# Performance work log

Hardware: AMD Instinct MI355X
Metric: run time of the kernel (lower is better)

Reference implementation:

```python
import jax, jax.numpy as jnp
import numpy as np

RAY_DIR = jnp.array([0.4395064455, 0.617598629942, 0.652231566745], dtype=jnp.float32)
TOL = 1e-7
CONTACT_THRESH = 25.0   # opt.contact_thresh
COLLISION_THRESH = 25.0  # opt.collision_thresh
BIG = 1e10


def mesh_contains(points, triangles, tri_valid):
    """Moller-Trumbore ray casting (fixed ray dir), parity test.
    points [B,P,3], triangles [B,T,3,3], tri_valid [B,T] -> exterior [B,P] bool."""
    v0, v1, v2 = triangles[:, :, 0, :], triangles[:, :, 1, :], triangles[:, :, 2, :]
    e1 = v1 - v0
    e2 = v2 - v0
    pvec = jnp.cross(jnp.broadcast_to(RAY_DIR, e2.shape), e2)          # [B,T,3]
    dets = jnp.sum(e1 * pvec, -1)                                      # [B,T]
    parallel = jnp.abs(dets) < TOL
    invdet = 1.0 / (dets + 0.1 * TOL)
    tvec = points[:, None, :, :] - v0[:, :, None, :]                   # [B,T,P,3]
    u = jnp.sum(tvec * pvec[:, :, None, :], -1) * invdet[:, :, None]   # [B,T,P]
    qvec = jnp.cross(tvec, e1[:, :, None, :])                          # [B,T,P,3]
    v = jnp.sum(qvec * RAY_DIR, -1) * invdet[:, :, None]
    t = jnp.sum(e2[:, :, None, :] * qvec, -1) * invdet[:, :, None]
    inter = (u > 0) & (u < 1) & (v > 0) & (u + v < 1) & (t > TOL)
    inter = inter & (~parallel & tri_valid)[:, :, None]
    n_hits = jnp.sum(inter.astype(jnp.int32), axis=1)                  # [B,P]
    return (n_hits % 2) == 0


def masked_mean_loss(vals, mask):
    m = mask.astype(vals.dtype)
    tot = m.sum()
    loss = jnp.where(tot > 0, (m * vals).sum() / jnp.maximum(tot, 1.0), 0.0)
    row = m.sum(1)
    losses = jnp.where(row > 0, (m * vals).sum(1) / jnp.maximum(row, 1.0), 0.0)
    return loss, losses


def setup_inputs() -> dict:
    key = jax.random.key(0)
    ks = jax.random.split(key, 6)
    B, Nh, Fh, No, Fo = 8, 778, 1538, 2000, 4000
    hand_verts = jax.random.normal(ks[0], (B, Nh, 3), dtype=jnp.float32)
    hand_faces = jax.random.randint(ks[1], (B, Fh, 3), 0, Nh, dtype=jnp.int32)
    obj_verts = jax.random.normal(ks[2], (B, No, 3), dtype=jnp.float32)
    obj_faces = jax.random.randint(ks[3], (B, Fo, 3), 0, 1200, dtype=jnp.int32)
    obj_vert_splits = 1200 + jax.random.randint(ks[4], (B,), 0, No - 1200 + 1, dtype=jnp.int32)
    obj_face_splits = 2400 + jax.random.randint(ks[5], (B,), 0, Fo - 2400 + 1, dtype=jnp.int32)
    return {"hand_verts": hand_verts, "hand_faces": hand_faces,
            "obj_verts": obj_verts, "obj_faces": obj_faces,
            "obj_vert_splits": obj_vert_splits, "obj_face_splits": obj_face_splits}


def reference(hand_verts, hand_faces, obj_verts, obj_faces, obj_vert_splits, obj_face_splits):
    B, Nh, _ = hand_verts.shape
    No = obj_verts.shape[1]
    Fo = obj_faces.shape[1]
    sg = jax.lax.stop_gradient

    # gather triangles (batched)
    hand_tri = jax.vmap(lambda v, f: v[f])(hand_verts, hand_faces)     # [B,Fh,3,3]
    obj_tri = jax.vmap(lambda v, f: v[f])(obj_verts, obj_faces)        # [B,Fo,3,3]

    face_valid = jnp.arange(Fo)[None, :] < obj_face_splits[:, None]    # [B,Fo]
    vert_valid = jnp.arange(No)[None, :] < obj_vert_splits[:, None]    # [B,No]

    # containment tests run on detached geometry (as in original)
    hand_tri_valid = jnp.ones(hand_tri.shape[:2], dtype=bool)
    exterior_obj = mesh_contains(sg(obj_verts), sg(hand_tri), hand_tri_valid)   # [B,No]
    exterior_hand = mesh_contains(sg(hand_verts), sg(obj_tri), face_valid)      # [B,Nh]

    penetr_o_mask = (~exterior_obj) & vert_valid
    penetr_h_mask = ~exterior_hand

    # ragged squared pairwise distances (bmm form of original), padded cols -> BIG
    rx = jnp.sum(hand_verts * hand_verts, -1)                          # [B,Nh]
    ry = jnp.sum(obj_verts * obj_verts, -1)                            # [B,No]
    zz = jnp.einsum('bnd,bmd->bnm', hand_verts, obj_verts)             # [B,Nh,No]
    dists = rx[:, :, None] + ry[:, None, :] - 2.0 * zz
    dists = jnp.where(vert_valid[:, None, :], dists, BIG)

    minoh_idxs = jnp.argmin(dists, axis=1)                             # [B,No]
    minho_idxs = jnp.argmin(dists, axis=2)                             # [B,Nh]

    results_close = jnp.take_along_axis(obj_verts, minho_idxs[:, :, None], axis=1)    # [B,Nh,3]
    results_o_close = jnp.take_along_axis(hand_verts, minoh_idxs[:, :, None], axis=1)  # [B,No,3]

    # contact_target == 'all'
    anchor_dists = jnp.sqrt(jnp.sum((results_close - hand_verts) ** 2, -1))    # [B,Nh]
    anchor_o_dist = jnp.sqrt(jnp.sum((results_o_close - obj_verts) ** 2, -1))  # [B,No]

    # contact_mode == 'dist_tanh' -> below_dist all ones
    contact_vals = CONTACT_THRESH * jnp.tanh(anchor_dists / CONTACT_THRESH)
    # collision_mode == 'dist_tanh'
    collision_vals = COLLISION_THRESH * jnp.tanh(anchor_dists / COLLISION_THRESH)
    collision_o_vals = COLLISION_THRESH * jnp.tanh(anchor_o_dist / COLLISION_THRESH)
    collision_o_vals = jnp.where(vert_valid, collision_o_vals, 0.0)

    # contact_zones == 'all'
    missed_mask = exterior_hand

    missed_loss, missed_losses = masked_mean_loss(contact_vals, missed_mask)
    penetr_h_loss, penetr_h_losses = masked_mean_loss(collision_vals, penetr_h_mask)
    penetr_o_loss, penetr_o_losses = masked_mean_loss(collision_o_vals, penetr_o_mask)
    penetr_loss = penetr_h_loss + penetr_o_loss
    penetr_losses = penetr_h_losses + penetr_o_losses

    return missed_loss, penetr_loss, missed_losses, penetr_losses
```

## Files before the change

### kernel.cpp

```cpp
#include <hip/hip_runtime.h>
#include <hip/hip_bf16.h>


#define RX 0.4395064455f
#define RY 0.617598629942f
#define RZ 0.652231566745f

#define MAXCHUNK_F4 512
#define PTS_PER_BLK 512

struct Params {
    const float* hand_verts; const int* hand_faces;
    const float* obj_verts;  const int* obj_faces;
    const int* ovsplit; const int* ofsplit;
    int* hitsA;
    int* hitsB;
    float* anchor_h; float* anchor_o; float* partials;
    unsigned int* done;
    float* out;
    int B, Nh, Fh, No, Fo;
    int pbA, CA, chunkA, blocksA;
    int pbB, CB, chunkB, blocksB;
};

__device__ __forceinline__ void tri_pre_one(const float* __restrict__ vb,
                                            const int* __restrict__ f,
                                            float4* o) {
#pragma clang fp contract(off)
    int i0 = f[0], i1 = f[1], i2 = f[2];
    float v0x = vb[i0*3+0], v0y = vb[i0*3+1], v0z = vb[i0*3+2];
    float v1x = vb[i1*3+0], v1y = vb[i1*3+1], v1z = vb[i1*3+2];
    float v2x = vb[i2*3+0], v2y = vb[i2*3+1], v2z = vb[i2*3+2];
    float e1x = v1x - v0x, e1y = v1y - v0y, e1z = v1z - v0z;
    float e2x = v2x - v0x, e2y = v2y - v0y, e2z = v2z - v0z;
    float px = RY*e2z - RZ*e2y;
    float py = RZ*e2x - RX*e2z;
    float pz = RX*e2y - RY*e2x;
    float det = (e1x*px + e1y*py) + e1z*pz;
    float invdet = 1.0f / (det + 1e-8f);
    bool valid = !(fabsf(det) < 1e-7f);
    o[0] = make_float4(v0x, v0y, v0z, invdet);
    o[1] = make_float4(e1x, e1y, e1z, valid ? 1.0f : 0.0f);
    o[2] = make_float4(e2x, e2y, e2z, 0.0f);
    o[3] = make_float4(px,  py,  pz,  0.0f);
}

__device__ __forceinline__ int mt_test(float qx, float qy, float qz,
                                       const float4& f0, const float4& f1,
                                       const float4& f2, const float4& f3) {
#pragma clang fp contract(off)
    float tvx = qx - f0.x, tvy = qy - f0.y, tvz = qz - f0.z;
    float u  = ((tvx*f3.x + tvy*f3.y) + tvz*f3.z) * f0.w;
    float qvx = tvy*f1.z - tvz*f1.y;
    float qvy = tvz*f1.x - tvx*f1.z;
    float qvz = tvx*f1.y - tvy*f1.x;
    float v  = ((qvx*RX + qvy*RY) + qvz*RZ) * f0.w;
    float tt = ((f2.x*qvx + f2.y*qvy) + f2.z*qvz) * f0.w;
    bool hit = (u > 0.0f) && (u < 1.0f) && (v > 0.0f) &&
               ((u + v) < 1.0f) && (tt > 1e-7f) && (f1.w != 0.0f);
    return hit ? 1 : 0;
}

__device__ __forceinline__ void raycast_vb(const Params& p, int vbid, int tid,
                                           float4* s_tri) {
#pragma clang fp contract(off)
    const float* pts; const float* tverts; const int* tfaces; int* slots;
    int P, T, Nv, c, pb, b, chunk, tlim, plim;
    if (vbid < p.blocksA) {
        int per_b = p.pbA * p.CA;
        b  = vbid / per_b;
        int r = vbid - b * per_b;
        c  = r / p.pbA;
        pb = r - c * p.pbA;
        pts = p.obj_verts; tverts = p.hand_verts; tfaces = p.hand_faces;
        slots = p.hitsA;
        P = p.No; T = p.Fh; Nv = p.Nh; chunk = p.chunkA;
        tlim = p.Fh; plim = min(p.No, p.ovsplit[b]);
    } else {
        int j = vbid - p.blocksA;
        int per_b = p.pbB * p.CB;
        b  = j / per_b;
        int r = j - b * per_b;
        c  = r / p.pbB;
        pb = r - c * p.pbB;
        pts = p.hand_verts; tverts = p.obj_verts; tfaces = p.obj_faces;
        slots = p.hitsB;
        P = p.Nh; T = p.Fo; Nv = p.No; chunk = p.chunkB;
        tlim = min(p.Fo, p.ofsplit[b]); plim = p.Nh;
    }

    int tStart = c * chunk;
    if (tStart >= tlim) return;
    if (pb * PTS_PER_BLK >= plim) return;
    int nTri = min(tStart + chunk, tlim) - tStart;

    if (tid < nTri) {
        int t = tStart + tid;
        tri_pre_one(tverts + (size_t)b * Nv * 3,
                    tfaces + ((size_t)b * T + t) * 3,
                    s_tri + (size_t)tid * 4);
    }

    int p1 = pb * PTS_PER_BLK + tid;
    int p2 = p1 + 256;
    bool act1 = p1 < plim, act2 = p2 < plim;
    float q1x = 0.f, q1y = 0.f, q1z = 0.f;
    float q2x = 0.f, q2y = 0.f, q2z = 0.f;
    if (act1) {
        const float* q = pts + ((size_t)b * P + p1) * 3;
        q1x = q[0]; q1y = q[1]; q1z = q[2];
    }
    if (act2) {
        const float* q = pts + ((size_t)b * P + p2) * 3;
        q2x = q[0]; q2y = q[1]; q2z = q[2];
    }
    __syncthreads();

    if (!act1) return;
    int cnt1 = 0, cnt2 = 0;
    for (int i = 0; i < nTri; ++i) {
        const float4 f0 = s_tri[(i<<2)+0];
        const float4 f1 = s_tri[(i<<2)+1];
        const float4 f2 = s_tri[(i<<2)+2];
        const float4 f3 = s_tri[(i<<2)+3];
        cnt1 += mt_test(q1x, q1y, q1z, f0, f1, f2, f3);
        cnt2 += mt_test(q2x, q2y, q2z, f0, f1, f2, f3);
    }
    int* base = slots + ((size_t)(c * p.B + b)) * P;
    base[p1] = cnt1;
    if (act2) base[p2] = cnt2;
}

__device__ __forceinline__ void min_one(const Params& p, int w, int lane) {
#pragma clang fp contract(off)
    int nHand = p.B * p.Nh;
    const float* refv; const float* loopv; int loopN; float* outp;
    if (w < nHand) {
        int b = w / p.Nh;
        int n = w - b * p.Nh;
        refv  = p.hand_verts + ((size_t)b * p.Nh + n) * 3;
        loopv = p.obj_verts + (size_t)b * p.No * 3;
        loopN = p.ovsplit[b];
        outp  = p.anchor_h + (size_t)b * p.Nh + n;
    } else {
        int j = w - nHand;
        int b = j / p.No;
        int m = j - b * p.No;
        if (m >= p.ovsplit[b]) return;
        refv  = p.obj_verts + ((size_t)b * p.No + m) * 3;
        loopv = p.hand_verts + (size_t)b * p.Nh * 3;
        loopN = p.Nh;
        outp  = p.anchor_o + (size_t)b * p.No + m;
    }
    float hx = refv[0], hy = refv[1], hz = refv[2];
    float rx = (hx*hx + hy*hy) + hz*hz;
    unsigned long long best = ~0ull;
    for (int m = lane; m < loopN; m += 64) {
        float ox = loopv[m*3+0], oy = loopv[m*3+1], oz = loopv[m*3+2];
        float ry = (ox*ox + oy*oy) + oz*oz;
        float zz = (hx*ox + hy*oy) + hz*oz;
        float d = (rx + ry) - 2.0f * zz;
        unsigned long long e = ((unsigned long long)__float_as_uint(d) << 32) | (unsigned)m;
        if (e < best) best = e;
    }
    for (int off = 32; off > 0; off >>= 1) {
        unsigned long long o = __shfl_xor(best, off, 64);
        if (o < best) best = o;
    }
    if (lane == 0) {
        int idx = (best == ~0ull) ? 0 : (int)(best & 0xffffffffu);
        const float* cv = loopv + (size_t)idx * 3;
        float dx = cv[0] - hx, dy = cv[1] - hy, dz = cv[2] - hz;
        *outp = sqrtf((dx*dx + dy*dy) + dz*dz);
    }
}

__global__ __launch_bounds__(256) void mega(Params p) {
    __shared__ float4 s_tri[MAXCHUNK_F4];
    const int tid = threadIdx.x;
    const int bid = blockIdx.x;
    if (bid == 0 && tid == 0) *p.done = 0u;
    const int nRay = p.blocksA + p.blocksB;
    if (bid < nRay) {
        raycast_vb(p, bid, tid, s_tri);
    } else {
        int w = (bid - nRay) * 4 + (tid >> 6);
        if (w < p.B * (p.Nh + p.No)) min_one(p, w, tid & 63);
    }
}

__global__ __launch_bounds__(1024) void reduce_fin(Params p) {
    const int b = blockIdx.x, tid = threadIdx.x;
    const int wave = tid >> 6, lane = tid & 63;
    float s0=0.f,s1=0.f,s2=0.f,s3=0.f,s4=0.f,s5=0.f;

    int tlimB = min(p.Fo, p.ofsplit[b]);
    int nCB = (tlimB + p.chunkB - 1) / p.chunkB;
    for (int n = tid; n < p.Nh; n += 1024) {
        int par = 0;
        for (int c = 0; c < nCB; ++c)
            par += p.hitsB[((size_t)(c * p.B + b)) * p.Nh + n];
        bool ext = (par & 1) == 0;
        float val = 25.0f * tanhf(p.anchor_h[(size_t)b*p.Nh + n] / 25.0f);
        if (ext) { s0 += val; s1 += 1.0f; } else { s2 += val; s3 += 1.0f; }
    }
    int split = p.ovsplit[b];
    for (int m = tid; m < split; m += 1024) {
        int par = 0;
        for (int c = 0; c < p.CA; ++c)
            par += p.hitsA[((size_t)(c * p.B + b)) * p.No + m];
        if (par & 1) {
            s4 += 25.0f * tanhf(p.anchor_o[(size_t)b*p.No + m] / 25.0f);
            s5 += 1.0f;
        }
    }
    for (int off = 32; off > 0; off >>= 1) {
        s0 += __shfl_xor(s0, off, 64);
        s1 += __shfl_xor(s1, off, 64);
        s2 += __shfl_xor(s2, off, 64);
        s3 += __shfl_xor(s3, off, 64);
        s4 += __shfl_xor(s4, off, 64);
        s5 += __shfl_xor(s5, off, 64);
    }
    __shared__ float red[16][6];
    __shared__ bool s_last;
    if (lane == 0) {
        red[wave][0]=s0; red[wave][1]=s1; red[wave][2]=s2;
        red[wave][3]=s3; red[wave][4]=s4; red[wave][5]=s5;
    }
    __syncthreads();
    if (tid == 0) {
        float t0=0.f,t1=0.f,t2=0.f,t3=0.f,t4=0.f,t5=0.f;
        for (int wv = 0; wv < 16; ++wv) {
            t0 += red[wv][0]; t1 += red[wv][1]; t2 += red[wv][2];
            t3 += red[wv][3]; t4 += red[wv][4]; t5 += red[wv][5];
        }
        p.out[2 + b]  = (t1 > 0.f) ? t0 / fmaxf(t1, 1.f) : 0.f;
        float ph      = (t3 > 0.f) ? t2 / fmaxf(t3, 1.f) : 0.f;
        float po      = (t5 > 0.f) ? t4 / fmaxf(t5, 1.f) : 0.f;
        p.out[10 + b] = ph + po;
        float* pp = p.partials + b * 6;
        pp[0]=t0; pp[1]=t1; pp[2]=t2; pp[3]=t3; pp[4]=t4; pp[5]=t5;
        __threadfence();
        unsigned int old = atomicAdd(p.done, 1u);
        s_last = (old == (unsigned int)(gridDim.x - 1));
    }
    __syncthreads();
    if (!s_last || tid != 0) return;
    __threadfence();
    float sm=0.f,cm=0.f,sph=0.f,cph=0.f,spo=0.f,cpo=0.f;
    for (int bb = 0; bb < p.B; ++bb) {
        const float* pp = p.partials + bb * 6;
        sm  += pp[0]; cm  += pp[1]; sph += pp[2];
        cph += pp[3]; spo += pp[4]; cpo += pp[5];
    }
    float missed = (cm  > 0.f) ? sm  / fmaxf(cm , 1.f) : 0.f;
    float ph     = (cph > 0.f) ? sph / fmaxf(cph, 1.f) : 0.f;
    float po     = (cpo > 0.f) ? spo / fmaxf(cpo, 1.f) : 0.f;
    p.out[0] = missed;
    p.out[1] = ph + po;
}

extern "C" void kernel_launch(void* const* d_in, const int* in_sizes, int n_in,
                              void* d_out, int out_size, void* d_ws, size_t ws_size,
                              hipStream_t stream) {
    Params p;
    p.hand_verts = (const float*)d_in[0];
    p.hand_faces = (const int*)d_in[1];
    p.obj_verts  = (const float*)d_in[2];
    p.obj_faces  = (const int*)d_in[3];
    p.ovsplit    = (const int*)d_in[4];
    p.ofsplit    = (const int*)d_in[5];
    p.out        = (float*)d_out;

    p.B  = in_sizes[4];
    p.Nh = in_sizes[0] / (3 * p.B);
    p.Fh = in_sizes[1] / (3 * p.B);
    p.No = in_sizes[2] / (3 * p.B);
    p.Fo = in_sizes[3] / (3 * p.B);

    p.CA = 16; p.CB = 32;
    p.chunkA = (p.Fh + p.CA - 1) / p.CA;
    p.chunkB = (p.Fo + p.CB - 1) / p.CB;
    p.pbA = (p.No + PTS_PER_BLK - 1) / PTS_PER_BLK;
    p.pbB = (p.Nh + PTS_PER_BLK - 1) / PTS_PER_BLK;
    p.blocksA = p.pbA * p.CA * p.B;
    p.blocksB = p.pbB * p.CB * p.B;

    char* ws = (char*)d_ws;
    size_t off = 0;
    auto alloc = [&](size_t bytes) -> void* {
        void* q = ws + off;
        off = (off + bytes + 255) & ~(size_t)255;
        return q;
    };
    p.hitsA    = (int*)   alloc((size_t)p.CA * p.B * p.No * sizeof(int));
    p.hitsB    = (int*)   alloc((size_t)p.CB * p.B * p.Nh * sizeof(int));
    p.anchor_h = (float*) alloc((size_t)p.B * p.Nh * sizeof(float));
    p.anchor_o = (float*) alloc((size_t)p.B * p.No * sizeof(float));
    p.partials = (float*) alloc((size_t)p.B * 6 * sizeof(float));
    p.done     = (unsigned int*)alloc(sizeof(unsigned int));

    int totalMin   = p.B * (p.Nh + p.No);
    int nMinBlocks = (totalMin + 3) / 4;
    int grid = p.blocksA + p.blocksB + nMinBlocks;

    mega<<<grid, 256, 0, stream>>>(p);
    reduce_fin<<<p.B, 1024, 0, stream>>>(p);
}
```

Before: 133.4 us.

## Fuse reduction into cooperative persistent kernel and retile raycast with more points per thread

Replaces the two-kernel launch with a single cooperative persistent kernel that loops over virtual blocks, then uses grid syncs to run a split per-batch reduction and the final loss computation. The raycast now packs triangle data into three float4s plus one scalar, folding the parallel flag into a zero invdet. Each thread tests four points instead of two, with smaller triangle chunks (more chunks). This is meant to remove a kernel launch and cut shared-memory traffic per triangle. The cost is grid-wide barrier overhead, limits on cooperative occupancy, and a larger partial-hit buffer to reduce.

```diff
diff --git a/kernel.cpp b/kernel.cpp
--- a/kernel.cpp
+++ b/kernel.cpp
@@ -1,13 +1,15 @@
 #include <hip/hip_runtime.h>
-#include <hip/hip_bf16.h>
+#include <hip/hip_cooperative_groups.h>
+
+namespace cg = cooperative_groups;
 
 
 #define RX 0.4395064455f
 #define RY 0.617598629942f
 #define RZ 0.652231566745f
 
-#define MAXCHUNK_F4 512
-#define PTS_PER_BLK 512
+#define MAXCHUNK 128
+#define PTS_PER_BLK 1024
 
 struct Params {
     const float* hand_verts; const int* hand_faces;
@@ -15,17 +17,17 @@
     const int* ovsplit; const int* ofsplit;
     int* hitsA;
     int* hitsB;
-    float* anchor_h; float* anchor_o; float* partials;
-    unsigned int* done;
+    float* anchor_h; float* anchor_o;
+    float* partials;
     float* out;
     int B, Nh, Fh, No, Fo;
-    int pbA, CA, chunkA, blocksA;
-    int pbB, CB, chunkB, blocksB;
+    int chunkA, chunkB, nChA, nChB;
+    int pbA, pbB, blocksA, blocksB, nMinBlk;
 };
 
 __device__ __forceinline__ void tri_pre_one(const float* __restrict__ vb,
                                             const int* __restrict__ f,
-                                            float4* o) {
+                                            float4* o, float* opz) {
 #pragma clang fp contract(off)
     int i0 = f[0], i1 = f[1], i2 = f[2];
     float v0x = vb[i0*3+0], v0y = vb[i0*3+1], v0z = vb[i0*3+2];
@@ -38,36 +40,36 @@
     float pz = RX*e2y - RY*e2x;
     float det = (e1x*px + e1y*py) + e1z*pz;
     float invdet = 1.0f / (det + 1e-8f);
-    bool valid = !(fabsf(det) < 1e-7f);
+    if (fabsf(det) < 1e-7f) invdet = 0.0f;
     o[0] = make_float4(v0x, v0y, v0z, invdet);
-    o[1] = make_float4(e1x, e1y, e1z, valid ? 1.0f : 0.0f);
-    o[2] = make_float4(e2x, e2y, e2z, 0.0f);
-    o[3] = make_float4(px,  py,  pz,  0.0f);
+    o[1] = make_float4(e1x, e1y, e1z, px);
+    o[2] = make_float4(e2x, e2y, e2z, py);
+    *opz = pz;
 }
 
 __device__ __forceinline__ int mt_test(float qx, float qy, float qz,
                                        const float4& f0, const float4& f1,
-                                       const float4& f2, const float4& f3) {
+                                       const float4& f2, float pz) {
 #pragma clang fp contract(off)
     float tvx = qx - f0.x, tvy = qy - f0.y, tvz = qz - f0.z;
-    float u  = ((tvx*f3.x + tvy*f3.y) + tvz*f3.z) * f0.w;
+    float u  = ((tvx*f1.w + tvy*f2.w) + tvz*pz) * f0.w;
     float qvx = tvy*f1.z - tvz*f1.y;
     float qvy = tvz*f1.x - tvx*f1.z;
     float qvz = tvx*f1.y - tvy*f1.x;
     float v  = ((qvx*RX + qvy*RY) + qvz*RZ) * f0.w;
     float tt = ((f2.x*qvx + f2.y*qvy) + f2.z*qvz) * f0.w;
     bool hit = (u > 0.0f) && (u < 1.0f) && (v > 0.0f) &&
-               ((u + v) < 1.0f) && (tt > 1e-7f) && (f1.w != 0.0f);
+               ((u + v) < 1.0f) && (tt > 1e-7f);
     return hit ? 1 : 0;
 }
 
 __device__ __forceinline__ void raycast_vb(const Params& p, int vbid, int tid,
-                                           float4* s_tri) {
+                                           float4* s_tri, float* s_pz) {
 #pragma clang fp contract(off)
     const float* pts; const float* tverts; const int* tfaces; int* slots;
     int P, T, Nv, c, pb, b, chunk, tlim, plim;
     if (vbid < p.blocksA) {
-        int per_b = p.pbA * p.CA;
+        int per_b = p.pbA * p.nChA;
         b  = vbid / per_b;
         int r = vbid - b * per_b;
         c  = r / p.pbA;
@@ -78,7 +80,7 @@
         tlim = p.Fh; plim = min(p.No, p.ovsplit[b]);
     } else {
         int j = vbid - p.blocksA;
-        int per_b = p.pbB * p.CB;
+        int per_b = p.pbB * p.nChB;
         b  = j / per_b;
         int r = j - b * per_b;
         c  = r / p.pbB;
@@ -98,37 +100,37 @@
         int t = tStart + tid;
         tri_pre_one(tverts + (size_t)b * Nv * 3,
                     tfaces + ((size_t)b * T + t) * 3,
-                    s_tri + (size_t)tid * 4);
+                    s_tri + (size_t)tid * 3, s_pz + tid);
     }
 
     int p1 = pb * PTS_PER_BLK + tid;
-    int p2 = p1 + 256;
-    bool act1 = p1 < plim, act2 = p2 < plim;
-    float q1x = 0.f, q1y = 0.f, q1z = 0.f;
-    float q2x = 0.f, q2y = 0.f, q2z = 0.f;
-    if (act1) {
-        const float* q = pts + ((size_t)b * P + p1) * 3;
-        q1x = q[0]; q1y = q[1]; q1z = q[2];
-    }
-    if (act2) {
-        const float* q = pts + ((size_t)b * P + p2) * 3;
-        q2x = q[0]; q2y = q[1]; q2z = q[2];
-    }
+    int p2 = p1 + 256, p3 = p1 + 512, p4 = p1 + 768;
+    bool act1 = p1 < plim, act2 = p2 < plim, act3 = p3 < plim, act4 = p4 < plim;
+    float q1x=0.f,q1y=0.f,q1z=0.f, q2x=0.f,q2y=0.f,q2z=0.f;
+    float q3x=0.f,q3y=0.f,q3z=0.f, q4x=0.f,q4y=0.f,q4z=0.f;
+    if (act1) { const float* q = pts + ((size_t)b*P + p1)*3; q1x=q[0]; q1y=q[1]; q1z=q[2]; }
+    if (act2) { const float* q = pts + ((size_t)b*P + p2)*3; q2x=q[0]; q2y=q[1]; q2z=q[2]; }
+    if (act3) { const float* q = pts + ((size_t)b*P + p3)*3; q3x=q[0]; q3y=q[1]; q3z=q[2]; }
+    if (act4) { const float* q = pts + ((size_t)b*P + p4)*3; q4x=q[0]; q4y=q[1]; q4z=q[2]; }
     __syncthreads();
 
     if (!act1) return;
-    int cnt1 = 0, cnt2 = 0;
+    int c1=0, c2=0, c3=0, c4=0;
     for (int i = 0; i < nTri; ++i) {
-        const float4 f0 = s_tri[(i<<2)+0];
-        const float4 f1 = s_tri[(i<<2)+1];
-        const float4 f2 = s_tri[(i<<2)+2];
-        const float4 f3 = s_tri[(i<<2)+3];
-        cnt1 += mt_test(q1x, q1y, q1z, f0, f1, f2, f3);
-        cnt2 += mt_test(q2x, q2y, q2z, f0, f1, f2, f3);
+        const float4 f0 = s_tri[i*3+0];
+        const float4 f1 = s_tri[i*3+1];
+        const float4 f2 = s_tri[i*3+2];
+        const float pz = s_pz[i];
+        c1 += mt_test(q1x,q1y,q1z, f0,f1,f2,pz);
+        if (act2) c2 += mt_test(q2x,q2y,q2z, f0,f1,f2,pz);
+        if (act3) c3 += mt_test(q3x,q3y,q3z, f0,f1,f2,pz);
+        if (act4) c4 += mt_test(q4x,q4y,q4z, f0,f1,f2,pz);
     }
     int* base = slots + ((size_t)(c * p.B + b)) * P;
-    base[p1] = cnt1;
-    if (act2) base[p2] = cnt2;
+    base[p1] = c1;
+    if (act2) base[p2] = c2;
+    if (act3) base[p3] = c3;
+    if (act4) base[p4] = c4;
 }
 
 __device__ __forceinline__ void min_one(const Params& p, int w, int lane) {
@@ -175,28 +177,16 @@
     }
 }
 
-__global__ __launch_bounds__(256) void mega(Params p) {
-    __shared__ float4 s_tri[MAXCHUNK_F4];
-    const int tid = threadIdx.x;
-    const int bid = blockIdx.x;
-    if (bid == 0 && tid == 0) *p.done = 0u;
-    const int nRay = p.blocksA + p.blocksB;
-    if (bid < nRay) {
-        raycast_vb(p, bid, tid, s_tri);
-    } else {
-        int w = (bid - nRay) * 4 + (tid >> 6);
-        if (w < p.B * (p.Nh + p.No)) min_one(p, w, tid & 63);
-    }
-}
-
-__global__ __launch_bounds__(1024) void reduce_fin(Params p) {
-    const int b = blockIdx.x, tid = threadIdx.x;
+__device__ __forceinline__ void reduce_part(const Params& p, int r, int tid) {
+    const int b    = r >> 2;
     const int wave = tid >> 6, lane = tid & 63;
+    const int wv   = (r & 3) * 4 + wave;
+    const int vt   = wv * 64 + lane;
     float s0=0.f,s1=0.f,s2=0.f,s3=0.f,s4=0.f,s5=0.f;
 
     int tlimB = min(p.Fo, p.ofsplit[b]);
     int nCB = (tlimB + p.chunkB - 1) / p.chunkB;
-    for (int n = tid; n < p.Nh; n += 1024) {
+    for (int n = vt; n < p.Nh; n += 1024) {
         int par = 0;
         for (int c = 0; c < nCB; ++c)
             par += p.hitsB[((size_t)(c * p.B + b)) * p.Nh + n];
@@ -205,9 +195,9 @@
         if (ext) { s0 += val; s1 += 1.0f; } else { s2 += val; s3 += 1.0f; }
     }
     int split = p.ovsplit[b];
-    for (int m = tid; m < split; m += 1024) {
+    for (int m = vt; m < split; m += 1024) {
         int par = 0;
-        for (int c = 0; c < p.CA; ++c)
+        for (int c = 0; c < p.nChA; ++c)
             par += p.hitsA[((size_t)(c * p.B + b)) * p.No + m];
         if (par & 1) {
             s4 += 25.0f * tanhf(p.anchor_o[(size_t)b*p.No + m] / 25.0f);
@@ -222,43 +212,67 @@
         s4 += __shfl_xor(s4, off, 64);
         s5 += __shfl_xor(s5, off, 64);
     }
-    __shared__ float red[16][6];
-    __shared__ bool s_last;
     if (lane == 0) {
-        red[wave][0]=s0; red[wave][1]=s1; red[wave][2]=s2;
-        red[wave][3]=s3; red[wave][4]=s4; red[wave][5]=s5;
-    }
-    __syncthreads();
-    if (tid == 0) {
-        float t0=0.f,t1=0.f,t2=0.f,t3=0.f,t4=0.f,t5=0.f;
-        for (int wv = 0; wv < 16; ++wv) {
-            t0 += red[wv][0]; t1 += red[wv][1]; t2 += red[wv][2];
-            t3 += red[wv][3]; t4 += red[wv][4]; t5 += red[wv][5];
+        float* q = p.partials + ((size_t)(b * 16 + wv)) * 6;
+        q[0]=s0; q[1]=s1; q[2]=s2; q[3]=s3; q[4]=s4; q[5]=s5;
+    }
+}
+
+__global__ __launch_bounds__(256, 4) void mega(Params p) {
+    __shared__ float4 s_tri[MAXCHUNK * 3];
+    __shared__ float  s_pz[MAXCHUNK];
+    __shared__ float  s_red[8][6];
+    const int tid = threadIdx.x;
+    const int nRay = p.blocksA + p.blocksB;
+    const int nVB  = nRay + p.nMinBlk;
+    const int totalMin = p.B * (p.Nh + p.No);
+
+    for (int vb = blockIdx.x; vb < nVB; vb += gridDim.x) {
+        if (vb < nRay) {
+            __syncthreads();
+            raycast_vb(p, vb, tid, s_tri, s_pz);
+        } else {
+            int w = (vb - nRay) * 4 + (tid >> 6);
+            if (w < totalMin) min_one(p, w, tid & 63);
         }
-        p.out[2 + b]  = (t1 > 0.f) ? t0 / fmaxf(t1, 1.f) : 0.f;
-        float ph      = (t3 > 0.f) ? t2 / fmaxf(t3, 1.f) : 0.f;
-        float po      = (t5 > 0.f) ? t4 / fmaxf(t5, 1.f) : 0.f;
-        p.out[10 + b] = ph + po;
-        float* pp = p.partials + b * 6;
-        pp[0]=t0; pp[1]=t1; pp[2]=t2; pp[3]=t3; pp[4]=t4; pp[5]=t5;
-        __threadfence();
-        unsigned int old = atomicAdd(p.done, 1u);
-        s_last = (old == (unsigned int)(gridDim.x - 1));
-    }
-    __syncthreads();
-    if (!s_last || tid != 0) return;
-    __threadfence();
-    float sm=0.f,cm=0.f,sph=0.f,cph=0.f,spo=0.f,cpo=0.f;
-    for (int bb = 0; bb < p.B; ++bb) {
-        const float* pp = p.partials + bb * 6;
-        sm  += pp[0]; cm  += pp[1]; sph += pp[2];
-        cph += pp[3]; spo += pp[4]; cpo += pp[5];
-    }
-    float missed = (cm  > 0.f) ? sm  / fmaxf(cm , 1.f) : 0.f;
-    float ph     = (cph > 0.f) ? sph / fmaxf(cph, 1.f) : 0.f;
-    float po     = (cpo > 0.f) ? spo / fmaxf(cpo, 1.f) : 0.f;
-    p.out[0] = missed;
-    p.out[1] = ph + po;
+    }
+
+    cg::this_grid().sync();
+
+    if ((int)blockIdx.x < p.B * 4) reduce_part(p, blockIdx.x, tid);
+
+    cg::this_grid().sync();
+
+    if (blockIdx.x == 0) {
+        if (tid < p.B && tid < 8) {
+            int b = tid;
+            float t0=0.f,t1=0.f,t2=0.f,t3=0.f,t4=0.f,t5=0.f;
+            for (int w2 = 0; w2 < 16; ++w2) {
+                const float* q = p.partials + ((size_t)(b * 16 + w2)) * 6;
+                t0 += q[0]; t1 += q[1]; t2 += q[2];
+                t3 += q[3]; t4 += q[4]; t5 += q[5];
+            }
+            p.out[2 + b]  = (t1 > 0.f) ? t0 / fmaxf(t1, 1.f) : 0.f;
+            float ph      = (t3 > 0.f) ? t2 / fmaxf(t3, 1.f) : 0.f;
+            float po      = (t5 > 0.f) ? t4 / fmaxf(t5, 1.f) : 0.f;
+            p.out[10 + b] = ph + po;
+            s_red[b][0]=t0; s_red[b][1]=t1; s_red[b][2]=t2;
+            s_red[b][3]=t3; s_red[b][4]=t4; s_red[b][5]=t5;
+        }
+        __syncthreads();
+        if (tid == 0) {
+            float sm=0.f,cm=0.f,sph=0.f,cph=0.f,spo=0.f,cpo=0.f;
+            for (int bb = 0; bb < p.B; ++bb) {
+                sm  += s_red[bb][0]; cm  += s_red[bb][1]; sph += s_red[bb][2];
+                cph += s_red[bb][3]; spo += s_red[bb][4]; cpo += s_red[bb][5];
+            }
+            float missed = (cm  > 0.f) ? sm  / fmaxf(cm , 1.f) : 0.f;
+            float ph     = (cph > 0.f) ? sph / fmaxf(cph, 1.f) : 0.f;
+            float po     = (cpo > 0.f) ? spo / fmaxf(cpo, 1.f) : 0.f;
+            p.out[0] = missed;
+            p.out[1] = ph + po;
+        }
+    }
 }
 
 extern "C" void kernel_launch(void* const* d_in, const int* in_sizes, int n_in,
@@ -279,13 +293,31 @@
     p.No = in_sizes[2] / (3 * p.B);
     p.Fo = in_sizes[3] / (3 * p.B);
 
-    p.CA = 16; p.CB = 32;
-    p.chunkA = (p.Fh + p.CA - 1) / p.CA;
-    p.chunkB = (p.Fo + p.CB - 1) / p.CB;
+    auto conf = [&](int CAt, int CBt, int& chA, int& chB, int& nA, int& nB) -> size_t {
+        chA = (p.Fh + CAt - 1) / CAt; if (chA < 1) chA = 1;
+        chB = (p.Fo + CBt - 1) / CBt; if (chB < 1) chB = 1;
+        nA = (p.Fh + chA - 1) / chA;
+        nB = (p.Fo + chB - 1) / chB;
+        auto pad = [](size_t x){ return (x + 255) & ~(size_t)255; };
+        size_t s = 0;
+        s += pad((size_t)nA * p.B * p.No * sizeof(int));
+        s += pad((size_t)nB * p.B * p.Nh * sizeof(int));
+        s += pad((size_t)p.B * p.Nh * sizeof(float));
+        s += pad((size_t)p.B * p.No * sizeof(float));
+        s += pad((size_t)p.B * 16 * 6 * sizeof(float));
+        return s;
+    };
+    int chA, chB, nA, nB;
+    size_t need = conf(32, 64, chA, chB, nA, nB);
+    if (need > ws_size || chA > MAXCHUNK || chB > MAXCHUNK)
+        (void)conf(16, 32, chA, chB, nA, nB);
+    p.chunkA = chA; p.chunkB = chB; p.nChA = nA; p.nChB = nB;
+
     p.pbA = (p.No + PTS_PER_BLK - 1) / PTS_PER_BLK;
     p.pbB = (p.Nh + PTS_PER_BLK - 1) / PTS_PER_BLK;
-    p.blocksA = p.pbA * p.CA * p.B;
-    p.blocksB = p.pbB * p.CB * p.B;
+    p.blocksA = p.pbA * p.nChA * p.B;
+    p.blocksB = p.pbB * p.nChB * p.B;
+    p.nMinBlk = (p.B * (p.Nh + p.No) + 3) / 4;
 
     char* ws = (char*)d_ws;
     size_t off = 0;
@@ -294,17 +326,33 @@
         off = (off + bytes + 255) & ~(size_t)255;
         return q;
     };
-    p.hitsA    = (int*)   alloc((size_t)p.CA * p.B * p.No * sizeof(int));
-    p.hitsB    = (int*)   alloc((size_t)p.CB * p.B * p.Nh * sizeof(int));
+    p.hitsA    = (int*)   alloc((size_t)p.nChA * p.B * p.No * sizeof(int));
+    p.hitsB    = (int*)   alloc((size_t)p.nChB * p.B * p.Nh * sizeof(int));
     p.anchor_h = (float*) alloc((size_t)p.B * p.Nh * sizeof(float));
     p.anchor_o = (float*) alloc((size_t)p.B * p.No * sizeof(float));
-    p.partials = (float*) alloc((size_t)p.B * 6 * sizeof(float));
-    p.done     = (unsigned int*)alloc(sizeof(unsigned int));
-
-    int totalMin   = p.B * (p.Nh + p.No);
-    int nMinBlocks = (totalMin + 3) / 4;
-    int grid = p.blocksA + p.blocksB + nMinBlocks;
-
-    mega<<<grid, 256, 0, stream>>>(p);
-    reduce_fin<<<p.B, 1024, 0, stream>>>(p);
-}
+    p.partials = (float*) alloc((size_t)p.B * 16 * 6 * sizeof(float));
+
+    static int cap = 0;
+    if (cap == 0) {
+        int mbpc = 0;
+        if (hipOccupancyMaxActiveBlocksPerMultiprocessor(&mbpc, (const void*)mega,
+                                                         256, 0) != hipSuccess ||
+            mbpc <= 0)
+            mbpc = 4;
+        int dev = 0; hipGetDevice(&dev);
+        hipDeviceProp_t prop;
+        int cus = 256;
+        if (hipGetDeviceProperties(&prop, dev) == hipSuccess &&
+            prop.multiProcessorCount > 0)
+            cus = prop.multiProcessorCount;
+        cap = cus * mbpc;
+    }
+    int nVB = p.blocksA + p.blocksB + p.nMinBlk;
+    int grid = (nVB < cap) ? nVB : cap;
+    int minGrid = p.B * 4;
+    if (grid < minGrid) grid = minGrid;
+
+    void* args[] = { &p };
+    hipLaunchCooperativeKernel((const void*)mega, dim3(grid), dim3(256),
+                               args, 0, stream);
+}
```

After: 318.3 us. 139% more time.
